# Performance work log

Measured on AMD Instinct MI355X. Metric: run time of the kernel, lower is better.

Reference implementation:

```python
import jax, jax.numpy as jnp
import numpy as np

N_EMBED = 1024
N_HEAD = 16
BLOCK_SIZE = 2048
ROPE_BASE = 10000.0


def _rope_cache():
    # theta uses n_embed (full model dim) as denominator, as in the source,
    # then is truncated to head_size//2 frequencies.
    hs_half = N_EMBED // N_HEAD // 2
    j = jnp.arange(N_EMBED // 2, dtype=jnp.float32)
    theta = jnp.power(ROPE_BASE, -2.0 * j / N_EMBED)
    seq_idx = jnp.arange(BLOCK_SIZE, dtype=jnp.float32)
    idx_theta = jnp.einsum('i,j->ij', seq_idx, theta)[:, :hs_half]  # [block, hs/2]
    return jnp.stack([jnp.cos(idx_theta), jnp.sin(idx_theta)], axis=-1)  # [block, hs/2, 2]


def _apply_rope(x, cache):
    # x: [B, nh, T, hs]. FAITHFUL to source: rope indexes its cache by dim-1,
    # which here is the HEAD dim (rope is called after transpose(1,2)).
    B, d1, d2, hs = x.shape
    rc = cache[:d1, :hs // 2]            # [d1, hs/2, 2]
    rc = rc[None, :, None, :, :]          # [1, d1, 1, hs/2, 2]
    x2 = x.reshape(B, d1, d2, hs // 2, 2)
    cos, sin = rc[..., 0], rc[..., 1]
    xr, xi = x2[..., 0], x2[..., 1]
    rot = jnp.stack([xr * cos - xi * sin, xi * cos + xr * sin], axis=-1)
    return rot.reshape(B, d1, d2, hs).astype(x.dtype)


def setup_inputs() -> dict:
    key = jax.random.key(0)
    ks = jax.random.split(key, 5)
    B, T, C = 2, 2048, N_EMBED
    return {
        'x': jax.random.normal(ks[0], (B, T, C), dtype=jnp.float32),
        'w_attn': jax.random.normal(ks[1], (C, 3 * C), dtype=jnp.float32) * 0.02,
        'b_attn': jax.random.normal(ks[2], (3 * C,), dtype=jnp.float32) * 0.02,
        'w_proj': jax.random.normal(ks[3], (C, C), dtype=jnp.float32) * 0.02,
        'b_proj': jax.random.normal(ks[4], (C,), dtype=jnp.float32) * 0.02,
    }


def reference(x, w_attn, b_attn, w_proj, b_proj):
    B, T, C = x.shape
    nh, hs = N_HEAD, C // N_HEAD
    qkv = x @ w_attn + b_attn                     # [B, T, 3C]
    q, k, v = jnp.split(qkv, 3, axis=-1)
    q = q.reshape(B, T, nh, hs).transpose(0, 2, 1, 3)  # [B, nh, T, hs]
    k = k.reshape(B, T, nh, hs).transpose(0, 2, 1, 3)
    v = v.reshape(B, T, nh, hs).transpose(0, 2, 1, 3)
    cache = _rope_cache()
    q = _apply_rope(q, cache)
    k = _apply_rope(k, cache)
    scale = 1.0 / jnp.sqrt(jnp.asarray(hs, dtype=q.dtype))
    scores = jnp.einsum('bhqd,bhkd->bhqk', q, k) * scale
    causal = jnp.tril(jnp.ones((T, T), dtype=bool))
    scores = jnp.where(causal[None, None], scores, jnp.finfo(scores.dtype).min)
    attn = jax.nn.softmax(scores, axis=-1)
    y = jnp.einsum('bhqk,bhkd->bhqd', attn, v)    # [B, nh, T, hs]
    y = y.transpose(0, 2, 1, 3).reshape(B, T, C)
    return y @ w_proj + b_proj
```

## Files before the change

kernel.cpp:

```cpp
#include <hip/hip_runtime.h>
#include <hip/hip_bf16.h>
#include <math.h>

#define TSEQ 2048
#define CEMB 1024
#define NHEAD 16
#define HS 64

typedef __attribute__((ext_vector_type(8))) short bf16x8;
typedef __attribute__((ext_vector_type(4))) float f32x4;

__device__ __forceinline__ void gload16(const void* g, void* l) {
    __builtin_amdgcn_global_load_lds(
        (const __attribute__((address_space(1))) unsigned int*)g,
        (__attribute__((address_space(3))) unsigned int*)l, 16, 0, 0);
}

#define SWZ(row, colb) (((((row) << 7) + (colb))) ^ (((row) & 7) << 4))

__global__ void rope_tbl_k(float* __restrict__ tbl) {
    int i = blockIdx.x * blockDim.x + threadIdx.x;
    if (i >= NHEAD * 32) return;
    int h = i >> 5, j = i & 31;
    double theta = pow(10000.0, -2.0 * (double)j / 1024.0);
    double ang = (double)h * theta;
    tbl[2 * i + 0] = (float)cos(ang);
    tbl[2 * i + 1] = (float)sin(ang);
}

__global__ __launch_bounds__(256) void cvt_bf16_k(const float* __restrict__ in,
                                                  __hip_bfloat16* __restrict__ out) {
    int i = (blockIdx.x * 256 + threadIdx.x) * 8;
    float4 a = *(const float4*)(in + i);
    float4 b = *(const float4*)(in + i + 4);
    union { bf16x8 v; __hip_bfloat16 h[8]; } pk;
    pk.h[0] = __float2bfloat16(a.x); pk.h[1] = __float2bfloat16(a.y);
    pk.h[2] = __float2bfloat16(a.z); pk.h[3] = __float2bfloat16(a.w);
    pk.h[4] = __float2bfloat16(b.x); pk.h[5] = __float2bfloat16(b.y);
    pk.h[6] = __float2bfloat16(b.z); pk.h[7] = __float2bfloat16(b.w);
    *(bf16x8*)(out + i) = pk.v;
}

__global__ __launch_bounds__(256) void transpose_bf16_k(const float* __restrict__ src,
                                                        __hip_bfloat16* __restrict__ dst,
                                                        int K, int N) {
    __shared__ float tile[32][33];
    int n0 = blockIdx.x * 32, k0 = blockIdx.y * 32;
    int tx = threadIdx.x & 31, ty = threadIdx.x >> 5;
#pragma unroll
    for (int i = 0; i < 32; i += 8)
        tile[ty + i][tx] = src[(size_t)(k0 + ty + i) * N + n0 + tx];
    __syncthreads();
#pragma unroll
    for (int i = 0; i < 32; i += 8)
        dst[(size_t)(n0 + ty + i) * K + k0 + tx] = __float2bfloat16(tile[tx][ty + i]);
}

__global__ __launch_bounds__(256) void qkv_mfma_k(
    const __hip_bfloat16* __restrict__ Xb, const __hip_bfloat16* __restrict__ Wt,
    const float* __restrict__ bias, const float* __restrict__ tbl,
    __hip_bfloat16* __restrict__ Qb, __hip_bfloat16* __restrict__ Kb,
    __hip_bfloat16* __restrict__ Vtb)
{
    __shared__ __hip_bfloat16 Al[2][128 * 32];
    __shared__ __hip_bfloat16 Bl[2][128 * 32];
    const int tid = threadIdx.x;
    const int lane = tid & 63, w = tid >> 6;
    const int lr = lane & 15, lg = lane >> 4;
    const int wm = w >> 1, wn = w & 1;
    const int n0 = blockIdx.x * 128;
    const int m0 = blockIdx.y * 128;
    const __hip_bfloat16* gA = Xb + (size_t)(m0 + (tid >> 2)) * CEMB + (tid & 3) * 8;
    const __hip_bfloat16* gB = Wt + (size_t)(n0 + (tid >> 2)) * CEMB + (tid & 3) * 8;
#define QSTAGE(buf, kk) do { \
        gload16(gA + (kk), &Al[buf][tid * 8]); \
        gload16(gA + 64 * CEMB + (kk), &Al[buf][2048 + tid * 8]); \
        gload16(gB + (kk), &Bl[buf][tid * 8]); \
        gload16(gB + 64 * CEMB + (kk), &Bl[buf][2048 + tid * 8]); } while (0)
    f32x4 acc[4][4] = {};
    QSTAGE(0, 0);
    __syncthreads();
    for (int k0 = 0; k0 < CEMB; k0 += 32) {
        const int cur = (k0 >> 5) & 1;
        if (k0 + 32 < CEMB) QSTAGE(cur ^ 1, k0 + 32);
        bf16x8 af[4], bfr[4];
#pragma unroll
        for (int mi = 0; mi < 4; ++mi)
            af[mi] = *(const bf16x8*)&Al[cur][(wm * 64 + mi * 16 + lr) * 32 + lg * 8];
#pragma unroll
        for (int ni = 0; ni < 4; ++ni)
            bfr[ni] = *(const bf16x8*)&Bl[cur][(wn * 64 + ni * 16 + lr) * 32 + lg * 8];
#pragma unroll
        for (int mi = 0; mi < 4; ++mi)
#pragma unroll
            for (int ni = 0; ni < 4; ++ni)
                acc[mi][ni] = __builtin_amdgcn_mfma_f32_16x16x32_bf16(af[mi], bfr[ni], acc[mi][ni], 0, 0, 0);
        __syncthreads();
    }
    const int sec = (n0 >> 10);
#pragma unroll
    for (int mi = 0; mi < 4; ++mi) {
#pragma unroll
        for (int ni = 0; ni < 4; ++ni) {
            const int gcol = n0 + wn * 64 + ni * 16 + lr;
            const int c63 = gcol & 63;
            const int h = (gcol & 1023) >> 6;
            const int j = c63 >> 1;
            const float cth = tbl[(h * 32 + j) * 2 + 0];
            const float sth = tbl[(h * 32 + j) * 2 + 1];
            const float bv = bias[gcol];
            const int growb = m0 + wm * 64 + mi * 16 + lg * 4;
            const int bb = growb >> 11;
            const int t0 = growb & 2047;
            if (sec == 2) {
                union { unsigned long long u; __hip_bfloat16 hh[4]; } pk;
#pragma unroll
                for (int r = 0; r < 4; ++r) pk.hh[r] = __float2bfloat16(acc[mi][ni][r] + bv);
                *(unsigned long long*)&Vtb[(((size_t)bb * NHEAD + h) * HS + c63) * TSEQ + t0] = pk.u;
            } else {
                const float sc = (sec == 0) ? 0.18033688011112042f : 1.0f;
                __hip_bfloat16* dst = (sec == 0) ? Qb : Kb;
#pragma unroll
                for (int r = 0; r < 4; ++r) {
                    float val = acc[mi][ni][r] + bv;
                    float prt = __shfl_xor(val, 1);
                    float rot = (lr & 1) ? (val * cth + prt * sth) : (val * cth - prt * sth);
                    dst[(((size_t)bb * NHEAD + h) * TSEQ + t0 + r) * HS + c63] = __float2bfloat16(rot * sc);
                }
            }
        }
    }
#undef QSTAGE
}

__global__ __launch_bounds__(256) void attn_k(
    const __hip_bfloat16* __restrict__ Q, const __hip_bfloat16* __restrict__ K,
    const __hip_bfloat16* __restrict__ Vt, __hip_bfloat16* __restrict__ Y)
{
    __shared__ __hip_bfloat16 KsBuf[2][64 * 64];
    __shared__ __hip_bfloat16 VsBuf[2][64 * 64];
    __shared__ __hip_bfloat16 Ps[4][16][72];
    const int tid = threadIdx.x;
    const int w = tid >> 6;
    const int lane = tid & 63;
    const int lr = lane & 15;
    const int lg = lane >> 4;
    const int id = blockIdx.x;
    const int bh = id & 31;
    const int qblk = id >> 5;
    const size_t bho = (size_t)bh * TSEQ * HS;
    const int qw = qblk * 64 + w * 16;

    const __hip_bfloat16* Kg = K + bho;
    const __hip_bfloat16* Vg = Vt + bho;
    int ko0, ko1, vo0, vo1;
    {
        int o0 = tid * 16, o1 = o0 + 4096;
        int L0 = o0 ^ (((o0 >> 7) & 7) << 4);
        int L1 = o1 ^ (((o1 >> 7) & 7) << 4);
        ko0 = (L0 >> 7) * HS + ((L0 & 127) >> 1);
        ko1 = (L1 >> 7) * HS + ((L1 & 127) >> 1);
        vo0 = (L0 >> 7) * TSEQ + ((L0 & 127) >> 1);
        vo1 = (L1 >> 7) * TSEQ + ((L1 & 127) >> 1);
    }
#define ASTAGE(buf, kt_) do { \
        const __hip_bfloat16* kg_ = Kg + (size_t)(kt_) * 64 * HS; \
        const __hip_bfloat16* vg_ = Vg + (size_t)(kt_) * 64; \
        char* kb_ = (char*)KsBuf[buf]; char* vb_ = (char*)VsBuf[buf]; \
        gload16(kg_ + ko0, kb_ + tid * 16); \
        gload16(kg_ + ko1, kb_ + 4096 + tid * 16); \
        gload16(vg_ + vo0, vb_ + tid * 16); \
        gload16(vg_ + vo1, vb_ + 4096 + tid * 16); } while (0)

    bf16x8 qa[2];
    {
        const __hip_bfloat16* qp = Q + bho + (size_t)(qw + lr) * HS + lg * 8;
        qa[0] = *(const bf16x8*)(qp);
        qa[1] = *(const bf16x8*)(qp + 32);
    }
    const bf16x8 ones = {0x3F80, 0x3F80, 0x3F80, 0x3F80, 0x3F80, 0x3F80, 0x3F80, 0x3F80};
    float mrow[4] = {-1e30f, -1e30f, -1e30f, -1e30f};
    f32x4 lacc = {};
    f32x4 o[4] = {};

    ASTAGE(0, 0);
    __syncthreads();
    for (int kt = 0; kt <= qblk; ++kt) {
        const int cur = kt & 1;
        if (kt < qblk) ASTAGE(cur ^ 1, kt + 1);
        char* KsB = (char*)KsBuf[cur];
        char* VsB = (char*)VsBuf[cur];
        f32x4 s[4] = {};
#pragma unroll
        for (int ct = 0; ct < 4; ++ct) {
#pragma unroll
            for (int kb = 0; kb < 2; ++kb) {
                bf16x8 kf = *(const bf16x8*)(KsB + SWZ(ct * 16 + lr, kb * 64 + lg * 16));
                s[ct] = __builtin_amdgcn_mfma_f32_16x16x32_bf16(qa[kb], kf, s[ct], 0, 0, 0);
            }
        }
        if (kt == qblk) {
#pragma unroll
            for (int ct = 0; ct < 4; ++ct) {
                int col = kt * 64 + ct * 16 + lr;
#pragma unroll
                for (int r = 0; r < 4; ++r) {
                    if (col > qw + lg * 4 + r) s[ct][r] = -1e30f;
                }
            }
        }
#pragma unroll
        for (int r = 0; r < 4; ++r) {
            float mx = fmaxf(fmaxf(s[0][r], s[1][r]), fmaxf(s[2][r], s[3][r]));
            mx = fmaxf(mx, __shfl_xor(mx, 1));
            mx = fmaxf(mx, __shfl_xor(mx, 2));
            mx = fmaxf(mx, __shfl_xor(mx, 4));
            mx = fmaxf(mx, __shfl_xor(mx, 8));
            float mn = fmaxf(mrow[r], mx);
            float alpha = __builtin_amdgcn_exp2f(mrow[r] - mn);
            mrow[r] = mn;
            lacc[r] *= alpha;
            o[0][r] *= alpha; o[1][r] *= alpha; o[2][r] *= alpha; o[3][r] *= alpha;
#pragma unroll
            for (int ct = 0; ct < 4; ++ct) {
                float p = __builtin_amdgcn_exp2f(s[ct][r] - mn);
                Ps[w][lg * 4 + r][ct * 16 + lr] = __float2bfloat16(p);
            }
        }
#pragma unroll
        for (int kc = 0; kc < 2; ++kc) {
            bf16x8 pa = *(const bf16x8*)&Ps[w][lr][kc * 32 + lg * 8];
            lacc = __builtin_amdgcn_mfma_f32_16x16x32_bf16(pa, ones, lacc, 0, 0, 0);
#pragma unroll
            for (int ht = 0; ht < 4; ++ht) {
                bf16x8 vb = *(const bf16x8*)(VsB + SWZ(ht * 16 + lr, kc * 64 + lg * 16));
                o[ht] = __builtin_amdgcn_mfma_f32_16x16x32_bf16(pa, vb, o[ht], 0, 0, 0);
            }
        }
        __syncthreads();
    }
    const int b = bh >> 4, h = bh & 15;
#pragma unroll
    for (int r = 0; r < 4; ++r) {
        float inv = 1.f / lacc[r];
        int q = qw + lg * 4 + r;
        __hip_bfloat16* yp = Y + ((size_t)b * TSEQ + q) * CEMB + h * HS + lr;
#pragma unroll
        for (int ht = 0; ht < 4; ++ht) yp[ht * 16] = __float2bfloat16(o[ht][r] * inv);
    }
#undef ASTAGE
}

__global__ __launch_bounds__(256) void proj_mfma_k(
    const __hip_bfloat16* __restrict__ Ab, const __hip_bfloat16* __restrict__ Wt,
    const float* __restrict__ bias, float* __restrict__ out)
{
    __shared__ __hip_bfloat16 Al[2][128 * 32];
    __shared__ __hip_bfloat16 Bl[2][128 * 32];
    const int tid = threadIdx.x;
    const int lane = tid & 63, w = tid >> 6;
    const int lr = lane & 15, lg = lane >> 4;
    const int wm = w >> 1, wn = w & 1;
    const int n0 = blockIdx.x * 128;
    const int m0 = blockIdx.y * 128;
    const __hip_bfloat16* gA = Ab + (size_t)(m0 + (tid >> 2)) * CEMB + (tid & 3) * 8;
    const __hip_bfloat16* gB = Wt + (size_t)(n0 + (tid >> 2)) * CEMB + (tid & 3) * 8;
#define PSTAGE(buf, kk) do { \
        gload16(gA + (kk), &Al[buf][tid * 8]); \
        gload16(gA + 64 * CEMB + (kk), &Al[buf][2048 + tid * 8]); \
        gload16(gB + (kk), &Bl[buf][tid * 8]); \
        gload16(gB + 64 * CEMB + (kk), &Bl[buf][2048 + tid * 8]); } while (0)
    f32x4 acc[4][4] = {};
    PSTAGE(0, 0);
    __syncthreads();
    for (int k0 = 0; k0 < CEMB; k0 += 32) {
        const int cur = (k0 >> 5) & 1;
        if (k0 + 32 < CEMB) PSTAGE(cur ^ 1, k0 + 32);
        bf16x8 af[4], bfr[4];
#pragma unroll
        for (int mi = 0; mi < 4; ++mi)
            af[mi] = *(const bf16x8*)&Al[cur][(wm * 64 + mi * 16 + lr) * 32 + lg * 8];
#pragma unroll
        for (int ni = 0; ni < 4; ++ni)
            bfr[ni] = *(const bf16x8*)&Bl[cur][(wn * 64 + ni * 16 + lr) * 32 + lg * 8];
#pragma unroll
        for (int mi = 0; mi < 4; ++mi)
#pragma unroll
            for (int ni = 0; ni < 4; ++ni)
                acc[mi][ni] = __builtin_amdgcn_mfma_f32_16x16x32_bf16(af[mi], bfr[ni], acc[mi][ni], 0, 0, 0);
        __syncthreads();
    }
#pragma unroll
    for (int mi = 0; mi < 4; ++mi) {
#pragma unroll
        for (int ni = 0; ni < 4; ++ni) {
            const int gcol = n0 + wn * 64 + ni * 16 + lr;
            const float bv = bias[gcol];
            const int growb = m0 + wm * 64 + mi * 16 + lg * 4;
#pragma unroll
            for (int r = 0; r < 4; ++r)
                out[(size_t)(growb + r) * CEMB + gcol] = acc[mi][ni][r] + bv;
        }
    }
#undef PSTAGE
}

extern "C" void kernel_launch(void* const* d_in, const int* in_sizes, int n_in,
                              void* d_out, int out_size, void* d_ws, size_t ws_size,
                              hipStream_t stream)
{
    const float* x      = (const float*)d_in[0];
    const float* w_attn = (const float*)d_in[1];
    const float* b_attn = (const float*)d_in[2];
    const float* w_proj = (const float*)d_in[3];
    const float* b_proj = (const float*)d_in[4];
    float* out = (float*)d_out;
    char* base = (char*)d_ws;

    const size_t MB = 1048576;
    float* tbl          = (float*)base;
    __hip_bfloat16* Xb  = (__hip_bfloat16*)(base + 4096);
    __hip_bfloat16* Wta = (__hip_bfloat16*)(base + 4096 + 8 * MB);
    __hip_bfloat16* Wpt = (__hip_bfloat16*)(base + 4096 + 14 * MB);
    __hip_bfloat16* Qb  = (__hip_bfloat16*)(base + 4096 + 16 * MB);
    __hip_bfloat16* Kb  = (__hip_bfloat16*)(base + 4096 + 24 * MB);
    __hip_bfloat16* Vtb = (__hip_bfloat16*)(base + 4096 + 32 * MB);
    __hip_bfloat16* Yb  = Xb;

    rope_tbl_k<<<1, 512, 0, stream>>>(tbl);
    cvt_bf16_k<<<2048, 256, 0, stream>>>(x, Xb);
    transpose_bf16_k<<<dim3(96, 32), 256, 0, stream>>>(w_attn, Wta, CEMB, 3 * CEMB);
    transpose_bf16_k<<<dim3(32, 32), 256, 0, stream>>>(w_proj, Wpt, CEMB, CEMB);
    qkv_mfma_k<<<dim3(24, 32), 256, 0, stream>>>(Xb, Wta, b_attn, tbl, Qb, Kb, Vtb);
    attn_k<<<1024, 256, 0, stream>>>(Qb, Kb, Vtb, Yb);
    proj_mfma_k<<<dim3(8, 32), 256, 0, stream>>>(Yb, Wpt, b_proj, out);
}
```

Baseline: 149.4 us.

## Rewrite attention kernel with 32x32 MFMA, register-resident P, and causal tile skipping

The attention kernel moves from four waves using 16x16x32 MFMA to two waves, each owning 32 query rows and using 32x32x16 MFMA. It computes S transposed so the probabilities stay in registers: they are packed to bf16 and exchanged across lane halves with shuffles, replacing the LDS round-trip and the ones-MFMA row sum. Wave 0 skips the fully masked upper half of the diagonal tile. Output is staged through a swizzled LDS tile so Y is written with 16-byte vector stores. The trade-off is fewer waves per block and more registers per wave, which may reduce occupancy and latency hiding.

After: 149.7 us. Within noise of the previous version (+0.2%).

```diff
diff --git a/kernel.cpp b/kernel.cpp
--- a/kernel.cpp
+++ b/kernel.cpp
@@ -9,6 +9,8 @@
 
 typedef __attribute__((ext_vector_type(8))) short bf16x8;
 typedef __attribute__((ext_vector_type(4))) float f32x4;
+typedef __attribute__((ext_vector_type(16))) float f32x16;
+typedef unsigned int u32;
 
 __device__ __forceinline__ void gload16(const void* g, void* l) {
     __builtin_amdgcn_global_load_lds(
@@ -16,7 +18,11 @@
         (__attribute__((address_space(3))) unsigned int*)l, 16, 0, 0);
 }
 
-#define SWZ(row, colb) (((((row) << 7) + (colb))) ^ (((row) & 7) << 4))
+__device__ __forceinline__ u32 pk2(float a, float b) {
+    union { u32 u; __hip_bfloat16 h[2]; } t;
+    t.h[0] = __float2bfloat16(a); t.h[1] = __float2bfloat16(b);
+    return t.u;
+}
 
 __global__ void rope_tbl_k(float* __restrict__ tbl) {
     int i = blockIdx.x * blockDim.x + threadIdx.x;
@@ -133,120 +139,188 @@
 #undef QSTAGE
 }
 
-__global__ __launch_bounds__(256) void attn_k(
+__global__ __launch_bounds__(128) void attn_k(
     const __hip_bfloat16* __restrict__ Q, const __hip_bfloat16* __restrict__ K,
     const __hip_bfloat16* __restrict__ Vt, __hip_bfloat16* __restrict__ Y)
 {
     __shared__ __hip_bfloat16 KsBuf[2][64 * 64];
     __shared__ __hip_bfloat16 VsBuf[2][64 * 64];
-    __shared__ __hip_bfloat16 Ps[4][16][72];
     const int tid = threadIdx.x;
     const int w = tid >> 6;
     const int lane = tid & 63;
-    const int lr = lane & 15;
-    const int lg = lane >> 4;
+    const int l31 = lane & 31;
+    const int hi = lane >> 5;
     const int id = blockIdx.x;
     const int bh = id & 31;
-    const int qblk = id >> 5;
+    const int qb = id >> 5;
     const size_t bho = (size_t)bh * TSEQ * HS;
-    const int qw = qblk * 64 + w * 16;
-
+    const int qw = qb * 64 + w * 32;
+
+    int srcK[4], srcV[4];
+#pragma unroll
+    for (int j = 0; j < 4; ++j) {
+        int L = (tid + 128 * j) * 16;
+        int row = L >> 7;
+        int ce = ((L & 127) ^ (((row ^ (row >> 3)) & 7) << 4)) >> 1;
+        srcK[j] = row * HS + ce;
+        srcV[j] = row * TSEQ + ce;
+    }
     const __hip_bfloat16* Kg = K + bho;
     const __hip_bfloat16* Vg = Vt + bho;
-    int ko0, ko1, vo0, vo1;
-    {
-        int o0 = tid * 16, o1 = o0 + 4096;
-        int L0 = o0 ^ (((o0 >> 7) & 7) << 4);
-        int L1 = o1 ^ (((o1 >> 7) & 7) << 4);
-        ko0 = (L0 >> 7) * HS + ((L0 & 127) >> 1);
-        ko1 = (L1 >> 7) * HS + ((L1 & 127) >> 1);
-        vo0 = (L0 >> 7) * TSEQ + ((L0 & 127) >> 1);
-        vo1 = (L1 >> 7) * TSEQ + ((L1 & 127) >> 1);
-    }
 #define ASTAGE(buf, kt_) do { \
         const __hip_bfloat16* kg_ = Kg + (size_t)(kt_) * 64 * HS; \
         const __hip_bfloat16* vg_ = Vg + (size_t)(kt_) * 64; \
         char* kb_ = (char*)KsBuf[buf]; char* vb_ = (char*)VsBuf[buf]; \
-        gload16(kg_ + ko0, kb_ + tid * 16); \
-        gload16(kg_ + ko1, kb_ + 4096 + tid * 16); \
-        gload16(vg_ + vo0, vb_ + tid * 16); \
-        gload16(vg_ + vo1, vb_ + 4096 + tid * 16); } while (0)
-
-    bf16x8 qa[2];
+        _Pragma("unroll") \
+        for (int j = 0; j < 4; ++j) { \
+            gload16(kg_ + srcK[j], kb_ + (tid + 128 * j) * 16); \
+            gload16(vg_ + srcV[j], vb_ + (tid + 128 * j) * 16); } } while (0)
+
+    bf16x8 qf[4];
     {
-        const __hip_bfloat16* qp = Q + bho + (size_t)(qw + lr) * HS + lg * 8;
-        qa[0] = *(const bf16x8*)(qp);
-        qa[1] = *(const bf16x8*)(qp + 32);
-    }
-    const bf16x8 ones = {0x3F80, 0x3F80, 0x3F80, 0x3F80, 0x3F80, 0x3F80, 0x3F80, 0x3F80};
-    float mrow[4] = {-1e30f, -1e30f, -1e30f, -1e30f};
-    f32x4 lacc = {};
-    f32x4 o[4] = {};
+        const __hip_bfloat16* qp = Q + bho + (size_t)(qw + l31) * HS + hi * 8;
+#pragma unroll
+        for (int kb = 0; kb < 4; ++kb) qf[kb] = *(const bf16x8*)(qp + kb * 16);
+    }
+    const int base0 = l31 * 128;
+    const int swz0 = ((l31 ^ (l31 >> 3)) & 7) << 4;
+    const int r32 = 32 + l31;
+    const int base1 = r32 * 128;
+    const int swz1 = ((r32 ^ (r32 >> 3)) & 7) << 4;
+
+    float mrow = -1e30f, lsum = 0.f;
+    f32x16 o0 = {}, o1 = {};
 
     ASTAGE(0, 0);
     __syncthreads();
-    for (int kt = 0; kt <= qblk; ++kt) {
+    for (int kt = 0; kt <= qb; ++kt) {
         const int cur = kt & 1;
-        if (kt < qblk) ASTAGE(cur ^ 1, kt + 1);
-        char* KsB = (char*)KsBuf[cur];
-        char* VsB = (char*)VsBuf[cur];
-        f32x4 s[4] = {};
-#pragma unroll
-        for (int ct = 0; ct < 4; ++ct) {
-#pragma unroll
-            for (int kb = 0; kb < 2; ++kb) {
-                bf16x8 kf = *(const bf16x8*)(KsB + SWZ(ct * 16 + lr, kb * 64 + lg * 16));
-                s[ct] = __builtin_amdgcn_mfma_f32_16x16x32_bf16(qa[kb], kf, s[ct], 0, 0, 0);
-            }
-        }
-        if (kt == qblk) {
-#pragma unroll
-            for (int ct = 0; ct < 4; ++ct) {
-                int col = kt * 64 + ct * 16 + lr;
-#pragma unroll
-                for (int r = 0; r < 4; ++r) {
-                    if (col > qw + lg * 4 + r) s[ct][r] = -1e30f;
+        if (kt < qb) ASTAGE(cur ^ 1, kt + 1);
+        const char* KsB = (const char*)KsBuf[cur];
+        const char* VsB = (const char*)VsBuf[cur];
+        const bool do1 = (w == 1) || (kt < qb);
+        f32x16 s0 = {}, s1 = {};
+#pragma unroll
+        for (int kb = 0; kb < 4; ++kb) {
+            bf16x8 kf = *(const bf16x8*)(KsB + base0 + ((kb * 32 + hi * 16) ^ swz0));
+            s0 = __builtin_amdgcn_mfma_f32_32x32x16_bf16(kf, qf[kb], s0, 0, 0, 0);
+        }
+        if (do1) {
+#pragma unroll
+            for (int kb = 0; kb < 4; ++kb) {
+                bf16x8 kf = *(const bf16x8*)(KsB + base1 + ((kb * 32 + hi * 16) ^ swz1));
+                s1 = __builtin_amdgcn_mfma_f32_32x32x16_bf16(kf, qf[kb], s1, 0, 0, 0);
+            }
+        }
+        if (kt == qb) {
+            if (w == 0) {
+#pragma unroll
+                for (int r = 0; r < 16; ++r) {
+                    int crow = (r & 3) + 8 * (r >> 2) + 4 * hi;
+                    if (crow > l31) s0[r] = -1e30f;
                 }
-            }
-        }
-#pragma unroll
-        for (int r = 0; r < 4; ++r) {
-            float mx = fmaxf(fmaxf(s[0][r], s[1][r]), fmaxf(s[2][r], s[3][r]));
-            mx = fmaxf(mx, __shfl_xor(mx, 1));
-            mx = fmaxf(mx, __shfl_xor(mx, 2));
-            mx = fmaxf(mx, __shfl_xor(mx, 4));
-            mx = fmaxf(mx, __shfl_xor(mx, 8));
-            float mn = fmaxf(mrow[r], mx);
-            float alpha = __builtin_amdgcn_exp2f(mrow[r] - mn);
-            mrow[r] = mn;
-            lacc[r] *= alpha;
-            o[0][r] *= alpha; o[1][r] *= alpha; o[2][r] *= alpha; o[3][r] *= alpha;
-#pragma unroll
-            for (int ct = 0; ct < 4; ++ct) {
-                float p = __builtin_amdgcn_exp2f(s[ct][r] - mn);
-                Ps[w][lg * 4 + r][ct * 16 + lr] = __float2bfloat16(p);
-            }
-        }
-#pragma unroll
-        for (int kc = 0; kc < 2; ++kc) {
-            bf16x8 pa = *(const bf16x8*)&Ps[w][lr][kc * 32 + lg * 8];
-            lacc = __builtin_amdgcn_mfma_f32_16x16x32_bf16(pa, ones, lacc, 0, 0, 0);
-#pragma unroll
-            for (int ht = 0; ht < 4; ++ht) {
-                bf16x8 vb = *(const bf16x8*)(VsB + SWZ(ht * 16 + lr, kc * 64 + lg * 16));
-                o[ht] = __builtin_amdgcn_mfma_f32_16x16x32_bf16(pa, vb, o[ht], 0, 0, 0);
+            } else {
+#pragma unroll
+                for (int r = 0; r < 16; ++r) {
+                    int crow = (r & 3) + 8 * (r >> 2) + 4 * hi;
+                    if (crow > l31) s1[r] = -1e30f;
+                }
+            }
+        }
+        float mx = s0[0];
+#pragma unroll
+        for (int r = 1; r < 16; ++r) mx = fmaxf(mx, s0[r]);
+        if (do1) {
+#pragma unroll
+            for (int r = 0; r < 16; ++r) mx = fmaxf(mx, s1[r]);
+        }
+        mx = fmaxf(mx, __shfl_xor(mx, 32));
+        const float mn = fmaxf(mrow, mx);
+        const float alpha = __builtin_amdgcn_exp2f(mrow - mn);
+        mrow = mn;
+        float ls = 0.f;
+#pragma unroll
+        for (int r = 0; r < 16; ++r) { s0[r] = __builtin_amdgcn_exp2f(s0[r] - mn); ls += s0[r]; }
+        if (do1) {
+#pragma unroll
+            for (int r = 0; r < 16; ++r) { s1[r] = __builtin_amdgcn_exp2f(s1[r] - mn); ls += s1[r]; }
+        }
+        ls += __shfl_xor(ls, 32);
+        lsum = lsum * alpha + ls;
+        o0 = o0 * alpha;
+        o1 = o1 * alpha;
+        union { u32 u[4]; bf16x8 v; } pa[4];
+        {
+            u32 w01 = pk2(s0[0], s0[1]),   w23 = pk2(s0[2], s0[3]);
+            u32 w45 = pk2(s0[4], s0[5]),   w67 = pk2(s0[6], s0[7]);
+            u32 w89 = pk2(s0[8], s0[9]),   wab = pk2(s0[10], s0[11]);
+            u32 wcd = pk2(s0[12], s0[13]), wef = pk2(s0[14], s0[15]);
+            u32 xa = __shfl_xor(hi ? w01 : w45, 32);
+            u32 xb = __shfl_xor(hi ? w23 : w67, 32);
+            u32 xc = __shfl_xor(hi ? w89 : wcd, 32);
+            u32 xd = __shfl_xor(hi ? wab : wef, 32);
+            if (hi == 0) {
+                pa[0].u[0] = w01; pa[0].u[1] = w23; pa[0].u[2] = xa;  pa[0].u[3] = xb;
+                pa[1].u[0] = w89; pa[1].u[1] = wab; pa[1].u[2] = xc;  pa[1].u[3] = xd;
+            } else {
+                pa[0].u[0] = xa;  pa[0].u[1] = xb;  pa[0].u[2] = w45; pa[0].u[3] = w67;
+                pa[1].u[0] = xc;  pa[1].u[1] = xd;  pa[1].u[2] = wcd; pa[1].u[3] = wef;
+            }
+        }
+        if (do1) {
+            u32 w01 = pk2(s1[0], s1[1]),   w23 = pk2(s1[2], s1[3]);
+            u32 w45 = pk2(s1[4], s1[5]),   w67 = pk2(s1[6], s1[7]);
+            u32 w89 = pk2(s1[8], s1[9]),   wab = pk2(s1[10], s1[11]);
+            u32 wcd = pk2(s1[12], s1[13]), wef = pk2(s1[14], s1[15]);
+            u32 xa = __shfl_xor(hi ? w01 : w45, 32);
+            u32 xb = __shfl_xor(hi ? w23 : w67, 32);
+            u32 xc = __shfl_xor(hi ? w89 : wcd, 32);
+            u32 xd = __shfl_xor(hi ? wab : wef, 32);
+            if (hi == 0) {
+                pa[2].u[0] = w01; pa[2].u[1] = w23; pa[2].u[2] = xa;  pa[2].u[3] = xb;
+                pa[3].u[0] = w89; pa[3].u[1] = wab; pa[3].u[2] = xc;  pa[3].u[3] = xd;
+            } else {
+                pa[2].u[0] = xa;  pa[2].u[1] = xb;  pa[2].u[2] = w45; pa[2].u[3] = w67;
+                pa[3].u[0] = xc;  pa[3].u[1] = xd;  pa[3].u[2] = wcd; pa[3].u[3] = wef;
+            }
+        }
+#pragma unroll
+        for (int ks = 0; ks < 2; ++ks) {
+            bf16x8 vf0 = *(const bf16x8*)(VsB + base0 + ((ks * 32 + hi * 16) ^ swz0));
+            o0 = __builtin_amdgcn_mfma_f32_32x32x16_bf16(vf0, pa[ks].v, o0, 0, 0, 0);
+            bf16x8 vf1 = *(const bf16x8*)(VsB + base1 + ((ks * 32 + hi * 16) ^ swz1));
+            o1 = __builtin_amdgcn_mfma_f32_32x32x16_bf16(vf1, pa[ks].v, o1, 0, 0, 0);
+        }
+        if (do1) {
+#pragma unroll
+            for (int ks = 2; ks < 4; ++ks) {
+                bf16x8 vf0 = *(const bf16x8*)(VsB + base0 + ((ks * 32 + hi * 16) ^ swz0));
+                o0 = __builtin_amdgcn_mfma_f32_32x32x16_bf16(vf0, pa[ks].v, o0, 0, 0, 0);
+                bf16x8 vf1 = *(const bf16x8*)(VsB + base1 + ((ks * 32 + hi * 16) ^ swz1));
+                o1 = __builtin_amdgcn_mfma_f32_32x32x16_bf16(vf1, pa[ks].v, o1, 0, 0, 0);
             }
         }
         __syncthreads();
     }
-    const int b = bh >> 4, h = bh & 15;
-#pragma unroll
-    for (int r = 0; r < 4; ++r) {
-        float inv = 1.f / lacc[r];
-        int q = qw + lg * 4 + r;
-        __hip_bfloat16* yp = Y + ((size_t)b * TSEQ + q) * CEMB + h * HS + lr;
-#pragma unroll
-        for (int ht = 0; ht < 4; ++ht) yp[ht * 16] = __float2bfloat16(o[ht][r] * inv);
+    __syncthreads();
+    {
+        char* T = (char*)KsBuf[0] + w * 4096;
+        const float inv = 1.f / lsum;
+        const int tsw = (l31 & 7) << 4;
+#pragma unroll
+        for (int r = 0; r < 16; ++r) {
+            int d0 = (r & 3) + 8 * (r >> 2) + 4 * hi;
+            *(__hip_bfloat16*)(T + base0 + ((d0 * 2) ^ tsw)) = __float2bfloat16(o0[r] * inv);
+            *(__hip_bfloat16*)(T + base0 + (((d0 + 32) * 2) ^ tsw)) = __float2bfloat16(o1[r] * inv);
+        }
+        const int b = bh >> 4, h = bh & 15;
+#pragma unroll
+        for (int p = 0; p < 4; ++p) {
+            int q = p * 8 + (lane >> 3);
+            int colb = ((lane & 7) * 16) ^ ((q & 7) << 4);
+            bf16x8 v = *(const bf16x8*)(T + q * 128 + colb);
+            *(bf16x8*)(Y + ((size_t)b * TSEQ + qw + q) * CEMB + h * HS + (lane & 7) * 8) = v;
+        }
     }
 #undef ASTAGE
 }
@@ -332,6 +406,6 @@
     transpose_bf16_k<<<dim3(96, 32), 256, 0, stream>>>(w_attn, Wta, CEMB, 3 * CEMB);
     transpose_bf16_k<<<dim3(32, 32), 256, 0, stream>>>(w_proj, Wpt, CEMB, CEMB);
     qkv_mfma_k<<<dim3(24, 32), 256, 0, stream>>>(Xb, Wta, b_attn, tbl, Qb, Kb, Vtb);
-    attn_k<<<1024, 256, 0, stream>>>(Qb, Kb, Vtb, Yb);
+    attn_k<<<1024, 128, 0, stream>>>(Qb, Kb, Vtb, Yb);
     proj_mfma_k<<<dim3(8, 32), 256, 0, stream>>>(Yb, Wpt, b_proj, out);
 }
```
